# Kernel tuning notes

Hardware: AMD Instinct MI355X
Metric: run time of the kernel (lower is better)

## Reference

```python
import jax, jax.numpy as jnp
import numpy as np

DIM = 2048
THRESH = 0.33

def _ternary(w):
    # sign() with dead zone: {-1, 0, +1}; detached from grad (matches torch.no_grad)
    return jax.lax.stop_gradient(jnp.where(jnp.abs(w) < THRESH, 0.0, jnp.sign(w)))

def _bitlinear(x, w, b):
    # F.linear(x, ternary_w, bias): x @ ternary_w.T + b
    return jnp.einsum('bsd,od->bso', x, _ternary(w)) + b

def setup_inputs() -> dict:
    key = jax.random.key(0)
    ks = jax.random.split(key, 6)
    B, S, D = 8, 2048, DIM
    x = jax.random.normal(ks[0], (B, S, D), dtype=jnp.float32)
    h_prev = jax.random.normal(ks[1], (B, S, D), dtype=jnp.float32)
    # BitLinear reset_parameters: uniform(-1, 1); bias zeros
    wf = jax.random.uniform(ks[2], (D, D), minval=-1.0, maxval=1.0, dtype=jnp.float32)
    wc = jax.random.uniform(ks[3], (D, D), minval=-1.0, maxval=1.0, dtype=jnp.float32)
    wg = jax.random.uniform(ks[4], (D, D), minval=-1.0, maxval=1.0, dtype=jnp.float32)
    wo = jax.random.uniform(ks[5], (D, D), minval=-1.0, maxval=1.0, dtype=jnp.float32)
    bf = jnp.zeros((D,), dtype=jnp.float32)
    bc = jnp.zeros((D,), dtype=jnp.float32)
    bg = jnp.zeros((D,), dtype=jnp.float32)
    bo = jnp.zeros((D,), dtype=jnp.float32)
    return {"x": x, "h_prev": h_prev, "wf": wf, "bf": bf, "wc": wc, "bc": bc,
            "wg": wg, "bg": bg, "wo": wo, "bo": bo}

def reference(x, h_prev, wf, bf, wc, bc, wg, bg, wo, bo):
    f = jax.nn.sigmoid(_bitlinear(x, wf, bf))
    c = jax.nn.silu(_bitlinear(x, wc, bc))
    h = f * h_prev + (1.0 - f) * c
    g = jax.nn.sigmoid(_bitlinear(x, wg, bg))
    o = _bitlinear(g * h, wo, bo)
    return (o, h)
```

## Files before the change

kernel.cpp:

```cpp
#include <hip/hip_runtime.h>
#include <hip/hip_bf16.h>
#include <cstdint>

#define DIM   2048
#define MROWS 16384
#define NH    64

typedef __bf16 bf16x8 __attribute__((ext_vector_type(8)));
typedef float  f32x4  __attribute__((ext_vector_type(4)));
typedef unsigned short u16;
typedef unsigned int   u32;

#define BARRIER() asm volatile("s_barrier" ::: "memory")
#define WAITVM(N) asm volatile("s_waitcnt vmcnt(" #N ")" ::: "memory")


__device__ __forceinline__ u16 ternary_bits(float w) {
    u32 u = __float_as_uint(w);
    u16 s = (u16)((u >> 16) & 0x8000u);
    return (__builtin_fabsf(w) < 0.33f) ? (u16)0 : (u16)(0x3F80u | s);
}

__device__ __forceinline__ u16 f2bf_rne(float f) {
    u32 u = __float_as_uint(f);
    u32 r = (u + 0x7FFFu + ((u >> 16) & 1u)) >> 16;
    return (u16)r;
}

__device__ __forceinline__ void gload16(const void* g, void* l) {
    __builtin_amdgcn_global_load_lds(
        (const __attribute__((address_space(1))) void*)g,
        (__attribute__((address_space(3))) void*)l,
        16, 0, 0);
}


__global__ void prep_weights(const float* __restrict__ wf, const float* __restrict__ wc,
                             const float* __restrict__ wg, const float* __restrict__ wo,
                             u16* __restrict__ out) {
    const float* srcs[4] = {wf, wc, wg, wo};
    const float* src = srcs[blockIdx.y];
    u16* dst = out + (size_t)blockIdx.y * (DIM * DIM);
    int e = (blockIdx.x * 256 + threadIdx.x) * 8;
    float4 v0 = *(const float4*)(src + e);
    float4 v1 = *(const float4*)(src + e + 4);
    ushort4 o0, o1;
    o0.x = ternary_bits(v0.x); o0.y = ternary_bits(v0.y);
    o0.z = ternary_bits(v0.z); o0.w = ternary_bits(v0.w);
    o1.x = ternary_bits(v1.x); o1.y = ternary_bits(v1.y);
    o1.z = ternary_bits(v1.z); o1.w = ternary_bits(v1.w);
    *(ushort4*)(dst + e)     = o0;
    *(ushort4*)(dst + e + 4) = o1;
}

__global__ void cast_x(const float* __restrict__ x, u16* __restrict__ xb) {
    size_t e = ((size_t)blockIdx.x * 256 + threadIdx.x) * 8;
    float4 v0 = *(const float4*)(x + e);
    float4 v1 = *(const float4*)(x + e + 4);
    ushort4 o0, o1;
    o0.x = f2bf_rne(v0.x); o0.y = f2bf_rne(v0.y);
    o0.z = f2bf_rne(v0.z); o0.w = f2bf_rne(v0.w);
    o1.x = f2bf_rne(v1.x); o1.y = f2bf_rne(v1.y);
    o1.z = f2bf_rne(v1.z); o1.w = f2bf_rne(v1.w);
    *(ushort4*)(xb + e)     = o0;
    *(ushort4*)(xb + e + 4) = o1;
}


__global__ __launch_bounds__(512) void gemm1(
    const u16* __restrict__ xb,
    const u16* __restrict__ wt,
    const float* __restrict__ bfv_, const float* __restrict__ bcv_, const float* __restrict__ bgv_,
    const float* __restrict__ hprev,
    float* __restrict__ hout,
    u16* __restrict__ gh)
{
    __shared__ __align__(16) u16 lds[4][16384];

    const int tid  = threadIdx.x;
    const int lane = tid & 63;
    const int wave = tid >> 6;
    const int wr   = wave >> 2;
    const int wcq  = wave & 3;

    const int bid  = blockIdx.x;
    const int swz  = (bid & 7) * 256 + (bid >> 3);
    const int brow = (swz & 127) * 128;
    const int bcol = (swz >> 7) * 128;

    const int row512 = tid >> 2;
    const int gc4    = (tid & 3) ^ ((tid >> 3) & 3);
    const int ldst   = tid * 8;

    const int fr  = lane & 15;
    const int hi  = lane >> 4;
    const int csw = (hi ^ ((fr >> 1) & 3)) * 8;

    f32x4 acc0[3][4] = {};
    f32x4 acc1[3][4] = {};

    const u16* aSrc  = xb + (size_t)(brow + row512) * DIM;
    const u16* bSrc0 = wt + (size_t)(bcol + row512) * DIM;
    const size_t WST = (size_t)DIM * DIM;

    auto issueHalf = [&](int slot, int k0) {
        gload16(aSrc + k0 + gc4 * 8,            (u16*)&lds[slot][ldst]);
        gload16(bSrc0 + 0 * WST + k0 + gc4 * 8, (u16*)&lds[slot][4096  + ldst]);
        gload16(bSrc0 + 1 * WST + k0 + gc4 * 8, (u16*)&lds[slot][8192  + ldst]);
        gload16(bSrc0 + 2 * WST + k0 + gc4 * 8, (u16*)&lds[slot][12288 + ldst]);
    };

    auto rdA = [&](const u16* sl, bf16x8 (&a)[4]) {
        #pragma unroll
        for (int mi = 0; mi < 4; ++mi)
            a[mi] = *(const bf16x8*)(sl + (wr * 64 + mi * 16 + fr) * 32 + csw);
    };
    auto rdB0 = [&](const u16* sl, bf16x8 (&b)[3]) {
        #pragma unroll
        for (int g = 0; g < 3; ++g)
            b[g] = *(const bf16x8*)(sl + 4096 + g * 4096 + (wcq * 32 + fr) * 32 + csw);
    };
    auto rdB1 = [&](const u16* sl, bf16x8 (&b)[3]) {
        #pragma unroll
        for (int g = 0; g < 3; ++g)
            b[g] = *(const bf16x8*)(sl + 4096 + g * 4096 + (wcq * 32 + 16 + fr) * 32 + csw);
    };
    auto mfmaC = [&](bf16x8 (&a)[4], bf16x8 (&b)[3], f32x4 (&c)[3][4]) {
        __builtin_amdgcn_s_setprio(1);
        #pragma unroll
        for (int g = 0; g < 3; ++g)
            #pragma unroll
            for (int mi = 0; mi < 4; ++mi)
                c[g][mi] = __builtin_amdgcn_mfma_f32_16x16x32_bf16(a[mi], b[g], c[g][mi], 0, 0, 0);
        __builtin_amdgcn_s_setprio(0);
    };

    bf16x8 aP[4], b0P[3], aQ[4], b0Q[3], b1[3];

    issueHalf(0, 0); issueHalf(1, 32); issueHalf(2, 64);
    WAITVM(8);
    BARRIER();
    rdA(&lds[0][0], aP); rdB0(&lds[0][0], b0P);

    auto step = [&](int j, bf16x8 (&aC)[4], bf16x8 (&b0C)[3],
                    bf16x8 (&aN)[4], bf16x8 (&b0N)[3]) {
        const u16* sl  = &lds[j & 3][0];
        const u16* sln = &lds[(j + 1) & 3][0];
        rdB1(sl, b1);
        issueHalf((j + 3) & 3, (j + 3) * 32);
        mfmaC(aC, b0C, acc0);
        WAITVM(8);
        BARRIER();
        rdA(sln, aN); rdB0(sln, b0N);
        mfmaC(aC, b1, acc1);
        BARRIER();
    };

    #pragma unroll 1
    for (int j = 0; j < NH - 4; j += 2) {
        step(j,     aP, b0P, aQ, b0Q);
        step(j + 1, aQ, b0Q, aP, b0P);
    }
    step(NH - 4, aP, b0P, aQ, b0Q);

    {
        const u16* sl  = &lds[(NH - 3) & 3][0];
        const u16* sln = &lds[(NH - 2) & 3][0];
        rdB1(sl, b1);
        mfmaC(aQ, b0Q, acc0);
        WAITVM(4);
        BARRIER();
        rdA(sln, aP); rdB0(sln, b0P);
        mfmaC(aQ, b1, acc1);
        BARRIER();
    }
    {
        const u16* sl  = &lds[(NH - 2) & 3][0];
        const u16* sln = &lds[(NH - 1) & 3][0];
        rdB1(sl, b1);
        mfmaC(aP, b0P, acc0);
        WAITVM(0);
        BARRIER();
        rdA(sln, aQ); rdB0(sln, b0Q);
        mfmaC(aP, b1, acc1);
        BARRIER();
    }
    {
        const u16* sl = &lds[(NH - 1) & 3][0];
        rdB1(sl, b1);
        mfmaC(aQ, b0Q, acc0);
        mfmaC(aQ, b1, acc1);
    }

    auto epi = [&](int ni, f32x4 (&c)[3][4]) {
        const int col = bcol + wcq * 32 + ni * 16 + fr;
        const float bfv = bfv_[col], bcv = bcv_[col], bgv = bgv_[col];
        #pragma unroll
        for (int mi = 0; mi < 4; ++mi) {
            #pragma unroll
            for (int j = 0; j < 4; ++j) {
                const int row = brow + wr * 64 + mi * 16 + hi * 4 + j;
                const size_t idx = (size_t)row * DIM + col;
                float pf = c[0][mi][j] + bfv;
                float pc = c[1][mi][j] + bcv;
                float pg = c[2][mi][j] + bgv;
                float f  = 1.f / (1.f + __expf(-pf));
                float cc = pc / (1.f + __expf(-pc));
                float g  = 1.f / (1.f + __expf(-pg));
                float hh = f * hprev[idx] + (1.f - f) * cc;
                hout[idx] = hh;
                gh[idx] = f2bf_rne(g * hh);
            }
        }
    };
    epi(0, acc0);
    epi(1, acc1);
}


__global__ __launch_bounds__(512) void gemm2(
    const u16* __restrict__ gh,
    const u16* __restrict__ wot,
    const float* __restrict__ bov_,
    float* __restrict__ oout)
{
    __shared__ __align__(16) u16 lds[3 * 16384];

    const int tid  = threadIdx.x;
    const int lane = tid & 63;
    const int wave = tid >> 6;
    const int wr   = wave >> 2;
    const int wcq  = wave & 3;

    const int bid  = blockIdx.x;
    const int swz  = (bid & 7) * 64 + (bid >> 3);
    const int brow = (swz & 63) * 256;
    const int bcol = (swz >> 6) * 256;

    const int srow = tid >> 2;
    const int gc4  = (tid & 3) ^ ((tid >> 3) & 3);
    const int ldst = tid * 8;

    const int fr  = lane & 15;
    const int hi  = lane >> 4;
    const int csw = (hi ^ ((fr >> 1) & 3)) * 8;

    f32x4 accL[8][2] = {};
    f32x4 accH[8][2] = {};

    const u16* aSrc0 = gh  + (size_t)(brow + srow) * DIM;
    const u16* aSrc1 = gh  + (size_t)(brow + 128 + srow) * DIM;
    const u16* bSrc0 = wot + (size_t)(bcol + srow) * DIM;
    const u16* bSrc1 = wot + (size_t)(bcol + 128 + srow) * DIM;

    auto issueA = [&](int so, int k0) {
        gload16(aSrc0 + k0 + gc4 * 8, (u16*)&lds[so + ldst]);
        gload16(aSrc1 + k0 + gc4 * 8, (u16*)&lds[so + 4096 + ldst]);
    };
    auto issueB = [&](int so, int k0) {
        gload16(bSrc0 + k0 + gc4 * 8, (u16*)&lds[so + 8192 + ldst]);
        gload16(bSrc1 + k0 + gc4 * 8, (u16*)&lds[so + 12288 + ldst]);
    };

    auto rdA = [&](int so, bf16x8 (&a)[8]) {
        #pragma unroll
        for (int mi = 0; mi < 8; ++mi)
            a[mi] = *(const bf16x8*)(&lds[so + (wr * 128 + mi * 16 + fr) * 32 + csw]);
    };
    auto rdBL = [&](int so, bf16x8 (&b)[2]) {
        #pragma unroll
        for (int jn = 0; jn < 2; ++jn)
            b[jn] = *(const bf16x8*)(&lds[so + 8192 + (wcq * 64 + jn * 16 + fr) * 32 + csw]);
    };
    auto rdBH = [&](int so, bf16x8 (&b)[2]) {
        #pragma unroll
        for (int jn = 0; jn < 2; ++jn)
            b[jn] = *(const bf16x8*)(&lds[so + 8192 + (wcq * 64 + (2 + jn) * 16 + fr) * 32 + csw]);
    };
    auto mfma2 = [&](bf16x8 (&a)[8], bf16x8 (&b)[2], f32x4 (&c)[8][2]) {
        __builtin_amdgcn_s_setprio(1);
        #pragma unroll
        for (int jn = 0; jn < 2; ++jn)
            #pragma unroll
            for (int mi = 0; mi < 8; ++mi)
                c[mi][jn] = __builtin_amdgcn_mfma_f32_16x16x32_bf16(a[mi], b[jn], c[mi][jn], 0, 0, 0);
        __builtin_amdgcn_s_setprio(0);
    };

    int so0 = 0, so1 = 16384, so2 = 32768;

    bf16x8 aP[8], bLP[2], aQ[8], bLQ[2], bH[2];

    issueA(so0, 0); issueB(so0, 0);
    issueA(so1, 32); issueB(so1, 32);
    WAITVM(4);
    BARRIER();
    rdA(so0, aP); rdBL(so0, bLP);

    auto step = [&](int h, bf16x8 (&aC)[8], bf16x8 (&bLC)[2],
                    bf16x8 (&aN)[8], bf16x8 (&bLN)[2]) {
        const int kn = (h + 2) * 32;
        rdBH(so0, bH);
        issueA(so2, kn);
        mfma2(aC, bLC, accL);
        WAITVM(2);
        BARRIER();
        rdA(so1, aN); rdBL(so1, bLN);
        issueB(so2, kn);
        mfma2(aC, bH, accH);
        BARRIER();
        int t = so0; so0 = so1; so1 = so2; so2 = t;
    };

    #pragma unroll 1
    for (int h = 0; h < NH - 2; h += 2) {
        step(h,     aP, bLP, aQ, bLQ);
        step(h + 1, aQ, bLQ, aP, bLP);
    }
    {
        rdBH(so0, bH);
        mfma2(aP, bLP, accL);
        WAITVM(0);
        BARRIER();
        rdA(so1, aQ); rdBL(so1, bLQ);
        mfma2(aP, bH, accH);
        BARRIER();
        int t = so0; so0 = so1; so1 = so2; so2 = t;
    }
    {
        rdBH(so0, bH);
        mfma2(aQ, bLQ, accL);
        mfma2(aQ, bH, accH);
    }

    auto epi2 = [&](int nbase, f32x4 (&c)[8][2]) {
        #pragma unroll
        for (int jn = 0; jn < 2; ++jn) {
            const int col = bcol + wcq * 64 + (nbase + jn) * 16 + fr;
            const float bov = bov_[col];
            #pragma unroll
            for (int mi = 0; mi < 8; ++mi)
                #pragma unroll
                for (int j = 0; j < 4; ++j)
                    oout[(size_t)(brow + wr * 128 + mi * 16 + hi * 4 + j) * DIM + col] = c[mi][jn][j] + bov;
        }
    };
    epi2(0, accL);
    epi2(2, accH);
}

extern "C" void kernel_launch(void* const* d_in, const int* in_sizes, int n_in,
                              void* d_out, int out_size, void* d_ws, size_t ws_size,
                              hipStream_t stream) {
    const float* x  = (const float*)d_in[0];
    const float* hp = (const float*)d_in[1];
    const float* wf = (const float*)d_in[2];
    const float* bf = (const float*)d_in[3];
    const float* wc = (const float*)d_in[4];
    const float* bc = (const float*)d_in[5];
    const float* wg = (const float*)d_in[6];
    const float* bg = (const float*)d_in[7];
    const float* wo = (const float*)d_in[8];
    const float* bo = (const float*)d_in[9];

    float* o_out = (float*)d_out;
    float* h_out = o_out + (size_t)MROWS * DIM;

    u16* w_t  = (u16*)d_ws;
    u16* x_bf = (u16*)((char*)d_ws + 33554432);
    u16* gh   = (u16*)((char*)d_ws + 100663296);

    prep_weights<<<dim3(2048, 4), 256, 0, stream>>>(wf, wc, wg, wo, w_t);
    cast_x<<<dim3(16384), 256, 0, stream>>>(x, x_bf);
    gemm1<<<dim3(2048), 512, 0, stream>>>(x_bf, w_t, bf, bc, bg, hp, h_out, gh);
    gemm2<<<dim3(512), 512, 0, stream>>>(gh, w_t + 3 * (size_t)DIM * DIM, bo, o_out);
}
```

Baseline: 715.1 us.

## Load A operand directly from global into registers, stage only B in LDS

The gemm1 kernel stops staging the activation tile in LDS. Each wave now loads its A fragments straight from global memory into registers one k-step ahead, and only the three ternary weight tiles go through the 4-slot LDS ring. This cuts LDS footprint and LDS read/write traffic, which may allow higher occupancy. In exchange, A is fetched redundantly by the four column waves, since there is no cross-wave sharing through LDS, and the wait counts now depend on the direct loads, so global latency is less hidden.

```diff
diff --git a/kernel.cpp b/kernel.cpp
--- a/kernel.cpp
+++ b/kernel.cpp
@@ -75,7 +75,7 @@
     float* __restrict__ hout,
     u16* __restrict__ gh)
 {
-    __shared__ __align__(16) u16 lds[4][16384];
+    __shared__ __align__(16) u16 lds[4][12288];
 
     const int tid  = threadIdx.x;
     const int lane = tid & 63;
@@ -99,31 +99,32 @@
     f32x4 acc0[3][4] = {};
     f32x4 acc1[3][4] = {};
 
-    const u16* aSrc  = xb + (size_t)(brow + row512) * DIM;
     const u16* bSrc0 = wt + (size_t)(bcol + row512) * DIM;
     const size_t WST = (size_t)DIM * DIM;
 
-    auto issueHalf = [&](int slot, int k0) {
-        gload16(aSrc + k0 + gc4 * 8,            (u16*)&lds[slot][ldst]);
-        gload16(bSrc0 + 0 * WST + k0 + gc4 * 8, (u16*)&lds[slot][4096  + ldst]);
-        gload16(bSrc0 + 1 * WST + k0 + gc4 * 8, (u16*)&lds[slot][8192  + ldst]);
-        gload16(bSrc0 + 2 * WST + k0 + gc4 * 8, (u16*)&lds[slot][12288 + ldst]);
-    };
-
-    auto rdA = [&](const u16* sl, bf16x8 (&a)[4]) {
+    const u16* aBase = xb + (size_t)(brow + wr * 64 + fr) * DIM + hi * 8;
+
+    auto loadA = [&](int kt, bf16x8 (&a)[4]) {
         #pragma unroll
         for (int mi = 0; mi < 4; ++mi)
-            a[mi] = *(const bf16x8*)(sl + (wr * 64 + mi * 16 + fr) * 32 + csw);
-    };
+            a[mi] = *(const bf16x8*)(aBase + (size_t)mi * 16 * DIM + kt);
+    };
+
+    auto issueB = [&](int slot, int k0) {
+        gload16(bSrc0 + 0 * WST + k0 + gc4 * 8, (u16*)&lds[slot][ldst]);
+        gload16(bSrc0 + 1 * WST + k0 + gc4 * 8, (u16*)&lds[slot][4096 + ldst]);
+        gload16(bSrc0 + 2 * WST + k0 + gc4 * 8, (u16*)&lds[slot][8192 + ldst]);
+    };
+
     auto rdB0 = [&](const u16* sl, bf16x8 (&b)[3]) {
         #pragma unroll
         for (int g = 0; g < 3; ++g)
-            b[g] = *(const bf16x8*)(sl + 4096 + g * 4096 + (wcq * 32 + fr) * 32 + csw);
+            b[g] = *(const bf16x8*)(sl + g * 4096 + (wcq * 32 + fr) * 32 + csw);
     };
     auto rdB1 = [&](const u16* sl, bf16x8 (&b)[3]) {
         #pragma unroll
         for (int g = 0; g < 3; ++g)
-            b[g] = *(const bf16x8*)(sl + 4096 + g * 4096 + (wcq * 32 + 16 + fr) * 32 + csw);
+            b[g] = *(const bf16x8*)(sl + g * 4096 + (wcq * 32 + 16 + fr) * 32 + csw);
     };
     auto mfmaC = [&](bf16x8 (&a)[4], bf16x8 (&b)[3], f32x4 (&c)[3][4]) {
         __builtin_amdgcn_s_setprio(1);
@@ -135,23 +136,25 @@
         __builtin_amdgcn_s_setprio(0);
     };
 
-    bf16x8 aP[4], b0P[3], aQ[4], b0Q[3], b1[3];
-
-    issueHalf(0, 0); issueHalf(1, 32); issueHalf(2, 64);
-    WAITVM(8);
+    bf16x8 aP[4], aQ[4], b0P[3], b0Q[3], b1[3];
+
+    issueB(0, 0); issueB(1, 32); issueB(2, 64);
+    loadA(0, aP);
+    WAITVM(0);
     BARRIER();
-    rdA(&lds[0][0], aP); rdB0(&lds[0][0], b0P);
+    rdB0(&lds[0][0], b0P);
 
     auto step = [&](int j, bf16x8 (&aC)[4], bf16x8 (&b0C)[3],
                     bf16x8 (&aN)[4], bf16x8 (&b0N)[3]) {
         const u16* sl  = &lds[j & 3][0];
         const u16* sln = &lds[(j + 1) & 3][0];
         rdB1(sl, b1);
-        issueHalf((j + 3) & 3, (j + 3) * 32);
+        loadA((j + 1) * 32, aN);
+        issueB((j + 3) & 3, (j + 3) * 32);
         mfmaC(aC, b0C, acc0);
-        WAITVM(8);
-        BARRIER();
-        rdA(sln, aN); rdB0(sln, b0N);
+        WAITVM(3);
+        BARRIER();
+        rdB0(sln, b0N);
         mfmaC(aC, b1, acc1);
         BARRIER();
     };
@@ -164,29 +167,31 @@
     step(NH - 4, aP, b0P, aQ, b0Q);
 
     {
-        const u16* sl  = &lds[(NH - 3) & 3][0];
-        const u16* sln = &lds[(NH - 2) & 3][0];
+        const u16* sl  = &lds[1][0];
+        const u16* sln = &lds[2][0];
         rdB1(sl, b1);
+        loadA(62 * 32, aP);
         mfmaC(aQ, b0Q, acc0);
-        WAITVM(4);
-        BARRIER();
-        rdA(sln, aP); rdB0(sln, b0P);
+        WAITVM(0);
+        BARRIER();
+        rdB0(sln, b0P);
         mfmaC(aQ, b1, acc1);
         BARRIER();
     }
     {
-        const u16* sl  = &lds[(NH - 2) & 3][0];
-        const u16* sln = &lds[(NH - 1) & 3][0];
+        const u16* sl  = &lds[2][0];
+        const u16* sln = &lds[3][0];
         rdB1(sl, b1);
+        loadA(63 * 32, aQ);
         mfmaC(aP, b0P, acc0);
         WAITVM(0);
         BARRIER();
-        rdA(sln, aQ); rdB0(sln, b0Q);
+        rdB0(sln, b0Q);
         mfmaC(aP, b1, acc1);
         BARRIER();
     }
     {
-        const u16* sl = &lds[(NH - 1) & 3][0];
+        const u16* sl = &lds[3][0];
         rdB1(sl, b1);
         mfmaC(aQ, b0Q, acc0);
         mfmaC(aQ, b1, acc1);
```

Result: slower. 1.144 ms (+60.0%).

## Restructure gemm1 to 4 waves with 64x64 per-wave tiles and double buffering

Applied to the files above, without the earlier changes.

The fused gate GEMM moves from 512 threads (8 waves, each owning a 64x32 output tile across three weights) to 256 threads (4 waves, each owning 64x64), with launch bounds asking for 2 blocks per CU. The 4-slot LDS ring with a hand-staggered software pipeline is replaced by a simple 2-slot double buffer that waits for all loads before a barrier every k-step. Each wave now holds 48 accumulator tiles, raising register pressure, and loads of the next stage overlap only one stage of MFMA work. The aim is more MFMA per LDS read and lower LDS footprint to allow two blocks per CU, at the risk of spills and weaker latency hiding.

```diff
diff --git a/kernel.cpp b/kernel.cpp
--- a/kernel.cpp
+++ b/kernel.cpp
@@ -67,7 +67,7 @@
 }
 
 
-__global__ __launch_bounds__(512) void gemm1(
+__global__ __launch_bounds__(256, 2) void gemm1(
     const u16* __restrict__ xb,
     const u16* __restrict__ wt,
     const float* __restrict__ bfv_, const float* __restrict__ bcv_, const float* __restrict__ bgv_,
@@ -75,39 +75,43 @@
     float* __restrict__ hout,
     u16* __restrict__ gh)
 {
-    __shared__ __align__(16) u16 lds[4][16384];
+    __shared__ __align__(16) u16 lds[2][16384];
 
     const int tid  = threadIdx.x;
     const int lane = tid & 63;
     const int wave = tid >> 6;
-    const int wr   = wave >> 2;
-    const int wcq  = wave & 3;
+    const int wr   = wave >> 1;
+    const int wcq  = wave & 1;
 
     const int bid  = blockIdx.x;
     const int swz  = (bid & 7) * 256 + (bid >> 3);
     const int brow = (swz & 127) * 128;
     const int bcol = (swz >> 7) * 128;
 
-    const int row512 = tid >> 2;
-    const int gc4    = (tid & 3) ^ ((tid >> 3) & 3);
-    const int ldst   = tid * 8;
+    const int row64 = tid >> 2;
+    const int gc4   = (tid & 3) ^ ((tid >> 3) & 3);
+    const int ldst  = tid * 8;
 
     const int fr  = lane & 15;
     const int hi  = lane >> 4;
     const int csw = (hi ^ ((fr >> 1) & 3)) * 8;
 
-    f32x4 acc0[3][4] = {};
-    f32x4 acc1[3][4] = {};
-
-    const u16* aSrc  = xb + (size_t)(brow + row512) * DIM;
-    const u16* bSrc0 = wt + (size_t)(bcol + row512) * DIM;
+    f32x4 acc[3][4][4] = {};
+
+    const u16* aSrc = xb + (size_t)(brow + row64) * DIM;
+    const u16* bSrc = wt + (size_t)(bcol + row64) * DIM;
     const size_t WST = (size_t)DIM * DIM;
 
     auto issueHalf = [&](int slot, int k0) {
-        gload16(aSrc + k0 + gc4 * 8,            (u16*)&lds[slot][ldst]);
-        gload16(bSrc0 + 0 * WST + k0 + gc4 * 8, (u16*)&lds[slot][4096  + ldst]);
-        gload16(bSrc0 + 1 * WST + k0 + gc4 * 8, (u16*)&lds[slot][8192  + ldst]);
-        gload16(bSrc0 + 2 * WST + k0 + gc4 * 8, (u16*)&lds[slot][12288 + ldst]);
+        gload16(aSrc + k0 + gc4 * 8,                        (u16*)&lds[slot][ldst]);
+        gload16(aSrc + (size_t)64 * DIM + k0 + gc4 * 8,     (u16*)&lds[slot][2048 + ldst]);
+        #pragma unroll
+        for (int g = 0; g < 3; ++g) {
+            gload16(bSrc + (size_t)g * WST + k0 + gc4 * 8,
+                    (u16*)&lds[slot][(2 + 2 * g) * 2048 + ldst]);
+            gload16(bSrc + (size_t)g * WST + (size_t)64 * DIM + k0 + gc4 * 8,
+                    (u16*)&lds[slot][(3 + 2 * g) * 2048 + ldst]);
+        }
     };
 
     auto rdA = [&](const u16* sl, bf16x8 (&a)[4]) {
@@ -115,95 +119,50 @@
         for (int mi = 0; mi < 4; ++mi)
             a[mi] = *(const bf16x8*)(sl + (wr * 64 + mi * 16 + fr) * 32 + csw);
     };
-    auto rdB0 = [&](const u16* sl, bf16x8 (&b)[3]) {
-        #pragma unroll
-        for (int g = 0; g < 3; ++g)
-            b[g] = *(const bf16x8*)(sl + 4096 + g * 4096 + (wcq * 32 + fr) * 32 + csw);
-    };
-    auto rdB1 = [&](const u16* sl, bf16x8 (&b)[3]) {
-        #pragma unroll
-        for (int g = 0; g < 3; ++g)
-            b[g] = *(const bf16x8*)(sl + 4096 + g * 4096 + (wcq * 32 + 16 + fr) * 32 + csw);
-    };
-    auto mfmaC = [&](bf16x8 (&a)[4], bf16x8 (&b)[3], f32x4 (&c)[3][4]) {
-        __builtin_amdgcn_s_setprio(1);
-        #pragma unroll
-        for (int g = 0; g < 3; ++g)
-            #pragma unroll
-            for (int mi = 0; mi < 4; ++mi)
-                c[g][mi] = __builtin_amdgcn_mfma_f32_16x16x32_bf16(a[mi], b[g], c[g][mi], 0, 0, 0);
-        __builtin_amdgcn_s_setprio(0);
-    };
-
-    bf16x8 aP[4], b0P[3], aQ[4], b0Q[3], b1[3];
-
-    issueHalf(0, 0); issueHalf(1, 32); issueHalf(2, 64);
-    WAITVM(8);
+
+    issueHalf(0, 0);
+    WAITVM(0);
     BARRIER();
-    rdA(&lds[0][0], aP); rdB0(&lds[0][0], b0P);
-
-    auto step = [&](int j, bf16x8 (&aC)[4], bf16x8 (&b0C)[3],
-                    bf16x8 (&aN)[4], bf16x8 (&b0N)[3]) {
-        const u16* sl  = &lds[j & 3][0];
-        const u16* sln = &lds[(j + 1) & 3][0];
-        rdB1(sl, b1);
-        issueHalf((j + 3) & 3, (j + 3) * 32);
-        mfmaC(aC, b0C, acc0);
-        WAITVM(8);
-        BARRIER();
-        rdA(sln, aN); rdB0(sln, b0N);
-        mfmaC(aC, b1, acc1);
-        BARRIER();
-    };
 
     #pragma unroll 1
-    for (int j = 0; j < NH - 4; j += 2) {
-        step(j,     aP, b0P, aQ, b0Q);
-        step(j + 1, aQ, b0Q, aP, b0P);
-    }
-    step(NH - 4, aP, b0P, aQ, b0Q);
-
-    {
-        const u16* sl  = &lds[(NH - 3) & 3][0];
-        const u16* sln = &lds[(NH - 2) & 3][0];
-        rdB1(sl, b1);
-        mfmaC(aQ, b0Q, acc0);
-        WAITVM(4);
-        BARRIER();
-        rdA(sln, aP); rdB0(sln, b0P);
-        mfmaC(aQ, b1, acc1);
-        BARRIER();
-    }
-    {
-        const u16* sl  = &lds[(NH - 2) & 3][0];
-        const u16* sln = &lds[(NH - 1) & 3][0];
-        rdB1(sl, b1);
-        mfmaC(aP, b0P, acc0);
-        WAITVM(0);
-        BARRIER();
-        rdA(sln, aQ); rdB0(sln, b0Q);
-        mfmaC(aP, b1, acc1);
-        BARRIER();
-    }
-    {
-        const u16* sl = &lds[(NH - 1) & 3][0];
-        rdB1(sl, b1);
-        mfmaC(aQ, b0Q, acc0);
-        mfmaC(aQ, b1, acc1);
-    }
-
-    auto epi = [&](int ni, f32x4 (&c)[3][4]) {
-        const int col = bcol + wcq * 32 + ni * 16 + fr;
+    for (int j = 0; j < NH; ++j) {
+        const u16* sl = &lds[j & 1][0];
+        bf16x8 a[4];
+        rdA(sl, a);
+        if (j + 1 < NH) issueHalf((j + 1) & 1, (j + 1) * 32);
+        #pragma unroll
+        for (int ni = 0; ni < 4; ++ni) {
+            bf16x8 b[3];
+            #pragma unroll
+            for (int g = 0; g < 3; ++g)
+                b[g] = *(const bf16x8*)(sl + 4096 + g * 4096 + (wcq * 64 + ni * 16 + fr) * 32 + csw);
+            __builtin_amdgcn_s_setprio(1);
+            #pragma unroll
+            for (int g = 0; g < 3; ++g)
+                #pragma unroll
+                for (int mi = 0; mi < 4; ++mi)
+                    acc[g][mi][ni] = __builtin_amdgcn_mfma_f32_16x16x32_bf16(a[mi], b[g], acc[g][mi][ni], 0, 0, 0);
+            __builtin_amdgcn_s_setprio(0);
+        }
+        if (j + 1 < NH) {
+            WAITVM(0);
+            BARRIER();
+        }
+    }
+
+    #pragma unroll
+    for (int ni = 0; ni < 4; ++ni) {
+        const int col = bcol + wcq * 64 + ni * 16 + fr;
         const float bfv = bfv_[col], bcv = bcv_[col], bgv = bgv_[col];
         #pragma unroll
         for (int mi = 0; mi < 4; ++mi) {
             #pragma unroll
-            for (int j = 0; j < 4; ++j) {
-                const int row = brow + wr * 64 + mi * 16 + hi * 4 + j;
+            for (int jj = 0; jj < 4; ++jj) {
+                const int row = brow + wr * 64 + mi * 16 + hi * 4 + jj;
                 const size_t idx = (size_t)row * DIM + col;
-                float pf = c[0][mi][j] + bfv;
-                float pc = c[1][mi][j] + bcv;
-                float pg = c[2][mi][j] + bgv;
+                float pf = acc[0][mi][ni][jj] + bfv;
+                float pc = acc[1][mi][ni][jj] + bcv;
+                float pg = acc[2][mi][ni][jj] + bgv;
                 float f  = 1.f / (1.f + __expf(-pf));
                 float cc = pc / (1.f + __expf(-pc));
                 float g  = 1.f / (1.f + __expf(-pg));
@@ -212,9 +171,7 @@
                 gh[idx] = f2bf_rne(g * hh);
             }
         }
-    };
-    epi(0, acc0);
-    epi(1, acc1);
+    }
 }
 
 
@@ -372,6 +329,6 @@
 
     prep_weights<<<dim3(2048, 4), 256, 0, stream>>>(wf, wc, wg, wo, w_t);
     cast_x<<<dim3(16384), 256, 0, stream>>>(x, x_bf);
-    gemm1<<<dim3(2048), 512, 0, stream>>>(x_bf, w_t, bf, bc, bg, hp, h_out, gh);
+    gemm1<<<dim3(2048), 256, 0, stream>>>(x_bf, w_t, bf, bc, bg, hp, h_out, gh);
     gemm2<<<dim3(512), 512, 0, stream>>>(gh, w_t + 3 * (size_t)DIM * DIM, bo, o_out);
 }
```

Result: no change. 701.5 us (-1.9%).
